# Kernel tuning notes

Hardware: AMD Instinct MI355X
Metric: run time of the kernel (lower is better)

## Reference

```python
import jax, jax.numpy as jnp
import numpy as np

N, IN_F, OUT_F = 8192, 4096, 4096
QMIN, QMAX = -128, 127  # int8 range for bitwidth 8


def setup_inputs() -> dict:
    key = jax.random.key(0)
    k1, k2, k3, k4 = jax.random.split(key, 4)
    x = jax.random.randint(k1, (N, IN_F), QMIN, QMAX + 1, dtype=jnp.int32).astype(jnp.int8)
    weight = jax.random.randint(k2, (OUT_F, IN_F), QMIN, QMAX + 1, dtype=jnp.int32).astype(jnp.int8)
    bias = jax.random.randint(k3, (OUT_F,), -1024, 1024, dtype=jnp.int32)
    weight_scale = jax.random.uniform(k4, (OUT_F,), dtype=jnp.float32, minval=0.001, maxval=0.02)
    input_scale = jnp.asarray([0.05], dtype=jnp.float32)
    output_scale = jnp.asarray([0.1], dtype=jnp.float32)
    output_zero_point = 0
    return {"x": x, "weight": weight, "bias": bias, "weight_scale": weight_scale,
            "input_scale": input_scale, "output_scale": output_scale,
            "output_zero_point": output_zero_point}


def reference(x, weight, bias, weight_scale, input_scale, output_scale, output_zero_point):
    # int32-accumulated GEMM with bias (CPU path of the torch module)
    acc = jnp.matmul(x.astype(jnp.int32), weight.astype(jnp.int32).T) + bias[None, :]  # [N, OUT_F] int32
    # fused dequant/requant epilogue
    scale_factor = (input_scale * weight_scale / output_scale)[None, :]  # [1, OUT_F]
    out = acc.astype(jnp.float32) * scale_factor + output_zero_point
    out = jnp.clip(jnp.round(out), QMIN, QMAX).astype(jnp.int8)
    return out
```

## Files before the change

### kernel.cpp

```cpp
#include <hip/hip_runtime.h>
#include <stdint.h>


#define M_DIM 8192
#define N_DIM 4096
#define K_DIM 4096
#define BM 256
#define BN 256
#define NKT2 (K_DIM / 32)
#define NBLK ((M_DIM / BM) * (N_DIM / BN))
#define ABUF (BM * 64)
#define BBUF (BN * 64)

using i32x4  = __attribute__((ext_vector_type(4))) int;
using i32x16 = __attribute__((ext_vector_type(16))) int;

typedef const __attribute__((address_space(1))) uint32_t* gptr_t;
typedef __attribute__((address_space(3))) uint32_t* lptr_t;

__device__ __forceinline__ void gload_lds16(const void* g, void* l) {
    __builtin_amdgcn_global_load_lds((gptr_t)g, (lptr_t)l, 16, 0, 0);
}

__device__ __forceinline__ int pack4(i32x4 v) {
    return (int)(((unsigned)v.x & 0xFFu) | (((unsigned)v.y & 0xFFu) << 8) |
                 (((unsigned)v.z & 0xFFu) << 16) | (((unsigned)v.w) << 24));
}

__global__ void pack_panels32_kernel(const int* __restrict__ src, int8_t* __restrict__ dst,
                                     int n_blocks) {
    int gid = blockIdx.x * blockDim.x + threadIdx.x;
    int blk = gid >> 6;
    int l = gid & 63;
    if (blk >= n_blocks) return;
    int rb = blk >> 7;
    int kt = blk & (NKT2 - 1);
    const i32x4* s4 = (const i32x4*)(src + (size_t)(rb * 32 + (l & 31)) * K_DIM
                                         + kt * 32 + (l >> 5) * 16);
    i32x4 o;
    o.x = pack4(s4[0]); o.y = pack4(s4[1]); o.z = pack4(s4[2]); o.w = pack4(s4[3]);
    *(i32x4*)(dst + (size_t)blk * 1024 + l * 16) = o;
}

#define MFMA32(a, b, c) __builtin_amdgcn_mfma_i32_32x32x32_i8((a), (b), (c), 0, 0, 0)

#define DSR(dst, base, off) \
    asm volatile("ds_read_b128 %0, %1 offset:%2" : "=&v"(dst) : "v"(base), "i"(off))

#define READ12(NS, SOFF)                                                        \
    DSR(fA[NS][0][0], aA, (SOFF) + 0);    DSR(fA[NS][0][1], aA, (SOFF) + 2048); \
    DSR(fA[NS][0][2], aA, (SOFF) + 4096); DSR(fA[NS][0][3], aA, (SOFF) + 6144); \
    DSR(fA[NS][1][0], aA, (SOFF) + 1024); DSR(fA[NS][1][1], aA, (SOFF) + 3072); \
    DSR(fA[NS][1][2], aA, (SOFF) + 5120); DSR(fA[NS][1][3], aA, (SOFF) + 7168); \
    DSR(fB[NS][0][0], aB, (SOFF) + 0);    DSR(fB[NS][0][1], aB, (SOFF) + 2048); \
    DSR(fB[NS][1][0], aB, (SOFF) + 1024); DSR(fB[NS][1][1], aB, (SOFF) + 3072);

#define MFMA_HALF(CS, K)                                                          \
    acc[0][0] = MFMA32(fA[CS][K][0], fB[CS][K][0], acc[0][0]);                    \
    acc[0][1] = MFMA32(fA[CS][K][0], fB[CS][K][1], acc[0][1]);                    \
    acc[1][0] = MFMA32(fA[CS][K][1], fB[CS][K][0], acc[1][0]);                    \
    acc[1][1] = MFMA32(fA[CS][K][1], fB[CS][K][1], acc[1][1]);                    \
    acc[2][0] = MFMA32(fA[CS][K][2], fB[CS][K][0], acc[2][0]);                    \
    acc[2][1] = MFMA32(fA[CS][K][2], fB[CS][K][1], acc[2][1]);                    \
    acc[3][0] = MFMA32(fA[CS][K][3], fB[CS][K][0], acc[3][0]);                    \
    acc[3][1] = MFMA32(fA[CS][K][3], fB[CS][K][1], acc[3][1]);

#define STAGE(SLOT)                                                     \
    gload_lds16(AgS,        ldsA + (SLOT) * ABUF + waoff);              \
    gload_lds16(AgS + 1024, ldsA + (SLOT) * ABUF + waoff + 1024);       \
    gload_lds16(BgS,        ldsB + (SLOT) * BBUF + waoff);              \
    gload_lds16(BgS + 1024, ldsB + (SLOT) * BBUF + waoff + 1024);       \
    AgS += 2048; BgS += 2048;

#define TILE_FULL(SLOT_STG, SOFF_NXT, NS, CS)                           \
  { STAGE(SLOT_STG)                                                     \
    asm volatile("s_waitcnt vmcnt(4)" ::: "memory");                    \
    __builtin_amdgcn_s_barrier();                                       \
    READ12(NS, SOFF_NXT)                                                \
    asm volatile("s_waitcnt lgkmcnt(12)" ::: "memory");                 \
    __builtin_amdgcn_sched_barrier(0);                                  \
    __builtin_amdgcn_s_setprio(1);                                      \
    MFMA_HALF(CS, 0)                                                    \
    MFMA_HALF(CS, 1)                                                    \
    __builtin_amdgcn_s_setprio(0); }

__global__ __launch_bounds__(512, 2)
void qgemm32_kernel(const int8_t* __restrict__ xp, const int8_t* __restrict__ wp,
                    const int* __restrict__ bias, const float* __restrict__ wscale,
                    const float* __restrict__ iscale, const float* __restrict__ oscale,
                    const int* __restrict__ zp, int* __restrict__ out) {
    extern __shared__ int8_t lds[];
    int8_t* ldsA = lds;
    int8_t* ldsB = lds + 4 * ABUF;

    const int tid  = threadIdx.x;
    const int wave = tid >> 6;
    const int lane = tid & 63;

    int b = blockIdx.x;
    int s = (b & 7) * (NBLK >> 3) + (b >> 3);
    const int bcol = (s & 15) * BN;
    const int brow = (s >> 4) * BM;

    const int wr = wave >> 2;
    const int wc = wave & 3;

    const int rb0 = brow >> 5;
    const int cb0 = bcol >> 5;
    const int8_t* AgS = xp + ((size_t)(rb0 + wave) * NKT2) * 1024 + lane * 16;
    const int8_t* BgS = wp + ((size_t)(cb0 + wave) * NKT2) * 1024 + lane * 16;
    const int waoff = wave * 2048;

    const unsigned aA = (unsigned)(uintptr_t)(ldsA + wr * 8192 + lane * 16);
    const unsigned aB = (unsigned)(uintptr_t)(ldsB + wc * 4096 + lane * 16);

    i32x16 acc[4][2] = {};
    i32x4 fA[2][2][4];
    i32x4 fB[2][2][2];

    STAGE(0)
    STAGE(1)
    asm volatile("s_waitcnt vmcnt(4)" ::: "memory");
    __builtin_amdgcn_s_barrier();
    READ12(0, 0)

    for (int i = 0; i < 15; ++i) {
        TILE_FULL(2, 16384, 1, 0)
        TILE_FULL(3, 32768, 0, 1)
        TILE_FULL(0, 49152, 1, 0)
        TILE_FULL(1,     0, 0, 1)
    }
    TILE_FULL(2, 16384, 1, 0)
    TILE_FULL(3, 32768, 0, 1)
    {
        asm volatile("s_waitcnt vmcnt(0)" ::: "memory");
        __builtin_amdgcn_s_barrier();
        READ12(1, 49152)
        asm volatile("s_waitcnt lgkmcnt(12)" ::: "memory");
        __builtin_amdgcn_sched_barrier(0);
        __builtin_amdgcn_s_setprio(1);
        MFMA_HALF(0, 0)
        MFMA_HALF(0, 1)
        __builtin_amdgcn_s_setprio(0);
    }
    asm volatile("s_waitcnt lgkmcnt(0)" ::: "memory");
    __builtin_amdgcn_sched_barrier(0);
    MFMA_HALF(1, 0)
    MFMA_HALF(1, 1)

    const float is_v = iscale[0];
    const float os_v = oscale[0];
    const float zpf = (float)zp[0];
    #pragma unroll
    for (int c = 0; c < 2; c++) {
        int col = bcol + wc * 64 + c * 32 + (lane & 31);
        float sf = (is_v * wscale[col]) / os_v;
        int bz = bias[col];
        #pragma unroll
        for (int r = 0; r < 4; r++) {
            int rowb = brow + wr * 128 + r * 32 + 4 * (lane >> 5);
            #pragma unroll
            for (int reg = 0; reg < 16; reg++) {
                int row = rowb + (reg & 3) + 8 * (reg >> 2);
                float v = (float)(acc[r][c][reg] + bz) * sf + zpf;
                v = rintf(v);
                v = fminf(fmaxf(v, -128.0f), 127.0f);
                out[(size_t)row * N_DIM + col] = (int)v;
            }
        }
    }
}

#define MFMA_I8(a, b, c) __builtin_amdgcn_mfma_i32_16x16x64_i8((a), (b), (c), 0, 0, 0)

__global__ void qgemm_fallback(const int* __restrict__ x32, const int* __restrict__ w32,
                               const int* __restrict__ bias, const float* __restrict__ wscale,
                               const float* __restrict__ iscale, const float* __restrict__ oscale,
                               const int* __restrict__ zp, int* __restrict__ out) {
    __shared__ int8_t As[128][64];
    __shared__ int8_t Bs[128][64];
    const int tid  = threadIdx.x;
    const int wave = tid >> 6;
    const int lane = tid & 63;
    int b = blockIdx.x;
    int s = (b & 7) * (gridDim.x >> 3) + (b >> 3);
    const int bcol = (s & 31) * 128;
    const int brow = (s >> 5) * 128;
    const int wr = wave >> 1;
    const int wc = wave & 1;
    i32x4 acc[4][4] = {};
    for (int kt = 0; kt < K_DIM; kt += 64) {
        int row = tid >> 1;
        int h = tid & 1;
        const i32x4* sa = (const i32x4*)(x32 + (size_t)(brow + row) * K_DIM + kt + h * 32);
        const i32x4* sb = (const i32x4*)(w32 + (size_t)(bcol + row) * K_DIM + kt + h * 32);
        int pa[8], pb[8];
        #pragma unroll
        for (int j = 0; j < 8; j++) { pa[j] = pack4(sa[j]); pb[j] = pack4(sb[j]); }
        *(i32x4*)&As[row][h * 32]      = *(i32x4*)&pa[0];
        *(i32x4*)&As[row][h * 32 + 16] = *(i32x4*)&pa[4];
        *(i32x4*)&Bs[row][h * 32]      = *(i32x4*)&pb[0];
        *(i32x4*)&Bs[row][h * 32 + 16] = *(i32x4*)&pb[4];
        __syncthreads();
        i32x4 a_frag[4], b_frag[4];
        #pragma unroll
        for (int m = 0; m < 4; m++)
            a_frag[m] = *(const i32x4*)&As[wr * 64 + m * 16 + (lane & 15)][(lane >> 4) * 16];
        #pragma unroll
        for (int n = 0; n < 4; n++)
            b_frag[n] = *(const i32x4*)&Bs[wc * 64 + n * 16 + (lane & 15)][(lane >> 4) * 16];
        #pragma unroll
        for (int m = 0; m < 4; m++)
            #pragma unroll
            for (int n = 0; n < 4; n++)
                acc[m][n] = MFMA_I8(a_frag[m], b_frag[n], acc[m][n]);
        __syncthreads();
    }
    const float is_v = iscale[0];
    const float os_v = oscale[0];
    const float zpf = (float)zp[0];
    #pragma unroll
    for (int n = 0; n < 4; n++) {
        int col = bcol + wc * 64 + n * 16 + (lane & 15);
        float sf = (is_v * wscale[col]) / os_v;
        int bz = bias[col];
        #pragma unroll
        for (int m = 0; m < 4; m++) {
            int row0 = brow + wr * 64 + m * 16 + (lane >> 4) * 4;
            #pragma unroll
            for (int r = 0; r < 4; r++) {
                float v = (float)(acc[m][n][r] + bz) * sf + zpf;
                v = rintf(v);
                v = fminf(fmaxf(v, -128.0f), 127.0f);
                out[(size_t)(row0 + r) * N_DIM + col] = (int)v;
            }
        }
    }
}

extern "C" void kernel_launch(void* const* d_in, const int* in_sizes, int n_in,
                              void* d_out, int out_size, void* d_ws, size_t ws_size,
                              hipStream_t stream) {
    const int*   x32    = (const int*)d_in[0];
    const int*   w32    = (const int*)d_in[1];
    const int*   bias   = (const int*)d_in[2];
    const float* wscale = (const float*)d_in[3];
    const float* iscale = (const float*)d_in[4];
    const float* oscale = (const float*)d_in[5];
    const int*   zp     = (const int*)d_in[6];
    int* out = (int*)d_out;

    const size_t need = (size_t)M_DIM * K_DIM + (size_t)N_DIM * K_DIM;
    const size_t lds_bytes = 4 * (size_t)(ABUF + BBUF);

    if (ws_size >= need) {
        int8_t* xp = (int8_t*)d_ws;
        int8_t* wp = xp + (size_t)M_DIM * K_DIM;
        const int nblkA = (M_DIM / 32) * NKT2;
        const int nblkB = (N_DIM / 32) * NKT2;
        pack_panels32_kernel<<<nblkA / 4, 256, 0, stream>>>(x32, xp, nblkA);
        pack_panels32_kernel<<<nblkB / 4, 256, 0, stream>>>(w32, wp, nblkB);
        (void)hipFuncSetAttribute((const void*)qgemm32_kernel,
                                  hipFuncAttributeMaxDynamicSharedMemorySize,
                                  (int)lds_bytes);
        qgemm32_kernel<<<NBLK, 512, lds_bytes, stream>>>(xp, wp, bias, wscale, iscale, oscale, zp, out);
    } else {
        qgemm_fallback<<<2048, 256, 0, stream>>>(x32, w32, bias, wscale, iscale, oscale, zp, out);
    }
}
```

Baseline: 183.3 us.

## Load B fragments straight from global into registers, bypassing LDS

The weight (B) operand is no longer staged through LDS. Each wave now issues global_load_dwordx4 directly into its fB fragment registers, one tile ahead, while A keeps its 4-slot global-to-LDS pipeline. This halves LDS use and drops the B ds_reads and their LDS bandwidth. In exchange, B global traffic is duplicated across the two wave rows that share a column. B load latency is hidden by only one tile of MFMA work, and register pressure rises.

```diff
diff --git a/kernel.cpp b/kernel.cpp
--- a/kernel.cpp
+++ b/kernel.cpp
@@ -10,7 +10,6 @@
 #define NKT2 (K_DIM / 32)
 #define NBLK ((M_DIM / BM) * (N_DIM / BN))
 #define ABUF (BM * 64)
-#define BBUF (BN * 64)
 
 using i32x4  = __attribute__((ext_vector_type(4))) int;
 using i32x16 = __attribute__((ext_vector_type(16))) int;
@@ -47,13 +46,20 @@
 #define DSR(dst, base, off) \
     asm volatile("ds_read_b128 %0, %1 offset:%2" : "=&v"(dst) : "v"(base), "i"(off))
 
-#define READ12(NS, SOFF)                                                        \
+#define GLB16(dst, addr, off) \
+    asm volatile("global_load_dwordx4 %0, %1, off offset:%2" \
+                 : "=&v"(dst) : "v"(addr), "i"(off))
+
+#define READ8(NS, SOFF)                                                         \
     DSR(fA[NS][0][0], aA, (SOFF) + 0);    DSR(fA[NS][0][1], aA, (SOFF) + 2048); \
     DSR(fA[NS][0][2], aA, (SOFF) + 4096); DSR(fA[NS][0][3], aA, (SOFF) + 6144); \
     DSR(fA[NS][1][0], aA, (SOFF) + 1024); DSR(fA[NS][1][1], aA, (SOFF) + 3072); \
-    DSR(fA[NS][1][2], aA, (SOFF) + 5120); DSR(fA[NS][1][3], aA, (SOFF) + 7168); \
-    DSR(fB[NS][0][0], aB, (SOFF) + 0);    DSR(fB[NS][0][1], aB, (SOFF) + 2048); \
-    DSR(fB[NS][1][0], aB, (SOFF) + 1024); DSR(fB[NS][1][1], aB, (SOFF) + 3072);
+    DSR(fA[NS][1][2], aA, (SOFF) + 5120); DSR(fA[NS][1][3], aA, (SOFF) + 7168);
+
+#define LOADB(NS)                                                       \
+    GLB16(fB[NS][0][0], Bg0, 0);    GLB16(fB[NS][1][0], Bg0, 1024);     \
+    GLB16(fB[NS][0][1], Bg1, 0);    GLB16(fB[NS][1][1], Bg1, 1024);     \
+    Bg0 += 2048; Bg1 += 2048;
 
 #define MFMA_HALF(CS, K)                                                          \
     acc[0][0] = MFMA32(fA[CS][K][0], fB[CS][K][0], acc[0][0]);                    \
@@ -65,19 +71,18 @@
     acc[3][0] = MFMA32(fA[CS][K][3], fB[CS][K][0], acc[3][0]);                    \
     acc[3][1] = MFMA32(fA[CS][K][3], fB[CS][K][1], acc[3][1]);
 
-#define STAGE(SLOT)                                                     \
+#define STAGE_A(SLOT)                                                   \
     gload_lds16(AgS,        ldsA + (SLOT) * ABUF + waoff);              \
     gload_lds16(AgS + 1024, ldsA + (SLOT) * ABUF + waoff + 1024);       \
-    gload_lds16(BgS,        ldsB + (SLOT) * BBUF + waoff);              \
-    gload_lds16(BgS + 1024, ldsB + (SLOT) * BBUF + waoff + 1024);       \
-    AgS += 2048; BgS += 2048;
+    AgS += 2048;
 
 #define TILE_FULL(SLOT_STG, SOFF_NXT, NS, CS)                           \
-  { STAGE(SLOT_STG)                                                     \
-    asm volatile("s_waitcnt vmcnt(4)" ::: "memory");                    \
+  { STAGE_A(SLOT_STG)                                                   \
+    LOADB(NS)                                                           \
+    asm volatile("s_waitcnt vmcnt(6)" ::: "memory");                    \
     __builtin_amdgcn_s_barrier();                                       \
-    READ12(NS, SOFF_NXT)                                                \
-    asm volatile("s_waitcnt lgkmcnt(12)" ::: "memory");                 \
+    READ8(NS, SOFF_NXT)                                                 \
+    asm volatile("s_waitcnt lgkmcnt(8)" ::: "memory");                  \
     __builtin_amdgcn_sched_barrier(0);                                  \
     __builtin_amdgcn_s_setprio(1);                                      \
     MFMA_HALF(CS, 0)                                                    \
@@ -91,7 +96,6 @@
                     const int* __restrict__ zp, int* __restrict__ out) {
     extern __shared__ int8_t lds[];
     int8_t* ldsA = lds;
-    int8_t* ldsB = lds + 4 * ABUF;
 
     const int tid  = threadIdx.x;
     const int wave = tid >> 6;
@@ -108,21 +112,23 @@
     const int rb0 = brow >> 5;
     const int cb0 = bcol >> 5;
     const int8_t* AgS = xp + ((size_t)(rb0 + wave) * NKT2) * 1024 + lane * 16;
-    const int8_t* BgS = wp + ((size_t)(cb0 + wave) * NKT2) * 1024 + lane * 16;
     const int waoff = wave * 2048;
 
+    const int8_t* Bg0 = wp + ((size_t)(cb0 + wc * 2)     * NKT2) * 1024 + lane * 16;
+    const int8_t* Bg1 = wp + ((size_t)(cb0 + wc * 2 + 1) * NKT2) * 1024 + lane * 16;
+
     const unsigned aA = (unsigned)(uintptr_t)(ldsA + wr * 8192 + lane * 16);
-    const unsigned aB = (unsigned)(uintptr_t)(ldsB + wc * 4096 + lane * 16);
 
     i32x16 acc[4][2] = {};
     i32x4 fA[2][2][4];
     i32x4 fB[2][2][2];
 
-    STAGE(0)
-    STAGE(1)
-    asm volatile("s_waitcnt vmcnt(4)" ::: "memory");
+    STAGE_A(0)
+    STAGE_A(1)
+    LOADB(0)
+    asm volatile("s_waitcnt vmcnt(0)" ::: "memory");
     __builtin_amdgcn_s_barrier();
-    READ12(0, 0)
+    READ8(0, 0)
 
     for (int i = 0; i < 15; ++i) {
         TILE_FULL(2, 16384, 1, 0)
@@ -133,16 +139,18 @@
     TILE_FULL(2, 16384, 1, 0)
     TILE_FULL(3, 32768, 0, 1)
     {
-        asm volatile("s_waitcnt vmcnt(0)" ::: "memory");
+        LOADB(1)
+        asm volatile("s_waitcnt vmcnt(4)" ::: "memory");
         __builtin_amdgcn_s_barrier();
-        READ12(1, 49152)
-        asm volatile("s_waitcnt lgkmcnt(12)" ::: "memory");
+        READ8(1, 49152)
+        asm volatile("s_waitcnt lgkmcnt(8)" ::: "memory");
         __builtin_amdgcn_sched_barrier(0);
         __builtin_amdgcn_s_setprio(1);
         MFMA_HALF(0, 0)
         MFMA_HALF(0, 1)
         __builtin_amdgcn_s_setprio(0);
     }
+    asm volatile("s_waitcnt vmcnt(0)" ::: "memory");
     asm volatile("s_waitcnt lgkmcnt(0)" ::: "memory");
     __builtin_amdgcn_sched_barrier(0);
     MFMA_HALF(1, 0)
@@ -251,7 +259,7 @@
     int* out = (int*)d_out;
 
     const size_t need = (size_t)M_DIM * K_DIM + (size_t)N_DIM * K_DIM;
-    const size_t lds_bytes = 4 * (size_t)(ABUF + BBUF);
+    const size_t lds_bytes = 4 * (size_t)ABUF;
 
     if (ws_size >= need) {
         int8_t* xp = (int8_t*)d_ws;
```

Result: slower. 187.2 us (+2.2%).

## Use 4 waves per block with 128x128 warp tiles instead of 8 waves

Applied to the files above, without the earlier changes.

Cuts the GEMM block from 8 waves to 4 and gives each wave a 128x128 output tile (4x4 MFMA 32x32 accumulators) instead of 128x64. Each wave now stages two 32-row panels of A and of B per K step, and the LDS slot addresses are precomputed. The goal is more MFMA work per LDS fragment read (16 reads feed 32 MFMAs versus 12 feeding 16). In exchange the accumulators double to 256 VGPRs per lane, there are fewer waves to hide latency, and the launch bound drops to one block per CU.

```diff
diff --git a/kernel.cpp b/kernel.cpp
--- a/kernel.cpp
+++ b/kernel.cpp
@@ -9,8 +9,7 @@
 #define BN 256
 #define NKT2 (K_DIM / 32)
 #define NBLK ((M_DIM / BM) * (N_DIM / BN))
-#define ABUF (BM * 64)
-#define BBUF (BN * 64)
+#define SLOT 16384
 
 using i32x4  = __attribute__((ext_vector_type(4))) int;
 using i32x16 = __attribute__((ext_vector_type(16))) int;
@@ -47,51 +46,65 @@
 #define DSR(dst, base, off) \
     asm volatile("ds_read_b128 %0, %1 offset:%2" : "=&v"(dst) : "v"(base), "i"(off))
 
-#define READ12(NS, SOFF)                                                        \
-    DSR(fA[NS][0][0], aA, (SOFF) + 0);    DSR(fA[NS][0][1], aA, (SOFF) + 2048); \
-    DSR(fA[NS][0][2], aA, (SOFF) + 4096); DSR(fA[NS][0][3], aA, (SOFF) + 6144); \
-    DSR(fA[NS][1][0], aA, (SOFF) + 1024); DSR(fA[NS][1][1], aA, (SOFF) + 3072); \
-    DSR(fA[NS][1][2], aA, (SOFF) + 5120); DSR(fA[NS][1][3], aA, (SOFF) + 7168); \
-    DSR(fB[NS][0][0], aB, (SOFF) + 0);    DSR(fB[NS][0][1], aB, (SOFF) + 2048); \
-    DSR(fB[NS][1][0], aB, (SOFF) + 1024); DSR(fB[NS][1][1], aB, (SOFF) + 3072);
-
-#define MFMA_HALF(CS, K)                                                          \
-    acc[0][0] = MFMA32(fA[CS][K][0], fB[CS][K][0], acc[0][0]);                    \
-    acc[0][1] = MFMA32(fA[CS][K][0], fB[CS][K][1], acc[0][1]);                    \
-    acc[1][0] = MFMA32(fA[CS][K][1], fB[CS][K][0], acc[1][0]);                    \
-    acc[1][1] = MFMA32(fA[CS][K][1], fB[CS][K][1], acc[1][1]);                    \
-    acc[2][0] = MFMA32(fA[CS][K][2], fB[CS][K][0], acc[2][0]);                    \
-    acc[2][1] = MFMA32(fA[CS][K][2], fB[CS][K][1], acc[2][1]);                    \
-    acc[3][0] = MFMA32(fA[CS][K][3], fB[CS][K][0], acc[3][0]);                    \
-    acc[3][1] = MFMA32(fA[CS][K][3], fB[CS][K][1], acc[3][1]);
-
-#define STAGE(SLOT)                                                     \
-    gload_lds16(AgS,        ldsA + (SLOT) * ABUF + waoff);              \
-    gload_lds16(AgS + 1024, ldsA + (SLOT) * ABUF + waoff + 1024);       \
-    gload_lds16(BgS,        ldsB + (SLOT) * BBUF + waoff);              \
-    gload_lds16(BgS + 1024, ldsB + (SLOT) * BBUF + waoff + 1024);       \
-    AgS += 2048; BgS += 2048;
-
-#define TILE_FULL(SLOT_STG, SOFF_NXT, NS, CS)                           \
-  { STAGE(SLOT_STG)                                                     \
-    asm volatile("s_waitcnt vmcnt(4)" ::: "memory");                    \
+#define READ16(NS, AB, BB)                                              \
+    DSR(fA[NS][0][0], AB, 0);    DSR(fA[NS][0][1], AB, 2048);           \
+    DSR(fA[NS][0][2], AB, 4096); DSR(fA[NS][0][3], AB, 6144);           \
+    DSR(fA[NS][1][0], AB, 1024); DSR(fA[NS][1][1], AB, 3072);           \
+    DSR(fA[NS][1][2], AB, 5120); DSR(fA[NS][1][3], AB, 7168);           \
+    DSR(fB[NS][0][0], BB, 0);    DSR(fB[NS][0][1], BB, 2048);           \
+    DSR(fB[NS][0][2], BB, 4096); DSR(fB[NS][0][3], BB, 6144);           \
+    DSR(fB[NS][1][0], BB, 1024); DSR(fB[NS][1][1], BB, 3072);           \
+    DSR(fB[NS][1][2], BB, 5120); DSR(fB[NS][1][3], BB, 7168);
+
+#define MFMA_K(CS, K)                                                   \
+    acc[0][0] = MFMA32(fA[CS][K][0], fB[CS][K][0], acc[0][0]);          \
+    acc[0][1] = MFMA32(fA[CS][K][0], fB[CS][K][1], acc[0][1]);          \
+    acc[0][2] = MFMA32(fA[CS][K][0], fB[CS][K][2], acc[0][2]);          \
+    acc[0][3] = MFMA32(fA[CS][K][0], fB[CS][K][3], acc[0][3]);          \
+    acc[1][0] = MFMA32(fA[CS][K][1], fB[CS][K][0], acc[1][0]);          \
+    acc[1][1] = MFMA32(fA[CS][K][1], fB[CS][K][1], acc[1][1]);          \
+    acc[1][2] = MFMA32(fA[CS][K][1], fB[CS][K][2], acc[1][2]);          \
+    acc[1][3] = MFMA32(fA[CS][K][1], fB[CS][K][3], acc[1][3]);          \
+    acc[2][0] = MFMA32(fA[CS][K][2], fB[CS][K][0], acc[2][0]);          \
+    acc[2][1] = MFMA32(fA[CS][K][2], fB[CS][K][1], acc[2][1]);          \
+    acc[2][2] = MFMA32(fA[CS][K][2], fB[CS][K][2], acc[2][2]);          \
+    acc[2][3] = MFMA32(fA[CS][K][2], fB[CS][K][3], acc[2][3]);          \
+    acc[3][0] = MFMA32(fA[CS][K][3], fB[CS][K][0], acc[3][0]);          \
+    acc[3][1] = MFMA32(fA[CS][K][3], fB[CS][K][1], acc[3][1]);          \
+    acc[3][2] = MFMA32(fA[CS][K][3], fB[CS][K][2], acc[3][2]);          \
+    acc[3][3] = MFMA32(fA[CS][K][3], fB[CS][K][3], acc[3][3]);
+
+#define STAGE8(S)                                                               \
+    gload_lds16(AgS,         ldsA + (S) * SLOT + (2 * wave) * 2048);            \
+    gload_lds16(AgS  + 1024, ldsA + (S) * SLOT + (2 * wave) * 2048 + 1024);     \
+    gload_lds16(AgS2,        ldsA + (S) * SLOT + (2 * wave + 1) * 2048);        \
+    gload_lds16(AgS2 + 1024, ldsA + (S) * SLOT + (2 * wave + 1) * 2048 + 1024); \
+    gload_lds16(BgS,         ldsB + (S) * SLOT + (2 * wave) * 2048);            \
+    gload_lds16(BgS  + 1024, ldsB + (S) * SLOT + (2 * wave) * 2048 + 1024);     \
+    gload_lds16(BgS2,        ldsB + (S) * SLOT + (2 * wave + 1) * 2048);        \
+    gload_lds16(BgS2 + 1024, ldsB + (S) * SLOT + (2 * wave + 1) * 2048 + 1024); \
+    AgS += 2048; AgS2 += 2048; BgS += 2048; BgS2 += 2048;
+
+#define TILE_FULL(SS, AB, BB, NS, CS)                                   \
+  { STAGE8(SS)                                                          \
+    asm volatile("s_waitcnt vmcnt(8)" ::: "memory");                    \
     __builtin_amdgcn_s_barrier();                                       \
-    READ12(NS, SOFF_NXT)                                                \
-    asm volatile("s_waitcnt lgkmcnt(12)" ::: "memory");                 \
+    READ16(NS, AB, BB)                                                  \
+    asm volatile("s_waitcnt lgkmcnt(15)" ::: "memory");                 \
     __builtin_amdgcn_sched_barrier(0);                                  \
     __builtin_amdgcn_s_setprio(1);                                      \
-    MFMA_HALF(CS, 0)                                                    \
-    MFMA_HALF(CS, 1)                                                    \
+    MFMA_K(CS, 0)                                                       \
+    MFMA_K(CS, 1)                                                       \
     __builtin_amdgcn_s_setprio(0); }
 
-__global__ __launch_bounds__(512, 2)
+__global__ __launch_bounds__(256, 1)
 void qgemm32_kernel(const int8_t* __restrict__ xp, const int8_t* __restrict__ wp,
                     const int* __restrict__ bias, const float* __restrict__ wscale,
                     const float* __restrict__ iscale, const float* __restrict__ oscale,
                     const int* __restrict__ zp, int* __restrict__ out) {
     extern __shared__ int8_t lds[];
     int8_t* ldsA = lds;
-    int8_t* ldsB = lds + 4 * ABUF;
+    int8_t* ldsB = lds + 4 * SLOT;
 
     const int tid  = threadIdx.x;
     const int wave = tid >> 6;
@@ -102,58 +115,61 @@
     const int bcol = (s & 15) * BN;
     const int brow = (s >> 4) * BM;
 
-    const int wr = wave >> 2;
-    const int wc = wave & 3;
+    const int wr = wave >> 1;
+    const int wc = wave & 1;
 
     const int rb0 = brow >> 5;
     const int cb0 = bcol >> 5;
-    const int8_t* AgS = xp + ((size_t)(rb0 + wave) * NKT2) * 1024 + lane * 16;
-    const int8_t* BgS = wp + ((size_t)(cb0 + wave) * NKT2) * 1024 + lane * 16;
-    const int waoff = wave * 2048;
-
-    const unsigned aA = (unsigned)(uintptr_t)(ldsA + wr * 8192 + lane * 16);
-    const unsigned aB = (unsigned)(uintptr_t)(ldsB + wc * 4096 + lane * 16);
-
-    i32x16 acc[4][2] = {};
+    const int8_t* AgS  = xp + ((size_t)(rb0 + 2 * wave)     * NKT2) * 1024 + lane * 16;
+    const int8_t* AgS2 = xp + ((size_t)(rb0 + 2 * wave + 1) * NKT2) * 1024 + lane * 16;
+    const int8_t* BgS  = wp + ((size_t)(cb0 + 2 * wave)     * NKT2) * 1024 + lane * 16;
+    const int8_t* BgS2 = wp + ((size_t)(cb0 + 2 * wave + 1) * NKT2) * 1024 + lane * 16;
+
+    const unsigned aA0 = (unsigned)(uintptr_t)(ldsA + wr * 8192 + lane * 16);
+    const unsigned aA1 = aA0 + SLOT, aA2 = aA0 + 2 * SLOT, aA3 = aA0 + 3 * SLOT;
+    const unsigned aB0 = (unsigned)(uintptr_t)(ldsB + wc * 8192 + lane * 16);
+    const unsigned aB1 = aB0 + SLOT, aB2 = aB0 + 2 * SLOT, aB3 = aB0 + 3 * SLOT;
+
+    i32x16 acc[4][4] = {};
     i32x4 fA[2][2][4];
-    i32x4 fB[2][2][2];
-
-    STAGE(0)
-    STAGE(1)
-    asm volatile("s_waitcnt vmcnt(4)" ::: "memory");
+    i32x4 fB[2][2][4];
+
+    STAGE8(0)
+    STAGE8(1)
+    asm volatile("s_waitcnt vmcnt(8)" ::: "memory");
     __builtin_amdgcn_s_barrier();
-    READ12(0, 0)
+    READ16(0, aA0, aB0)
 
     for (int i = 0; i < 15; ++i) {
-        TILE_FULL(2, 16384, 1, 0)
-        TILE_FULL(3, 32768, 0, 1)
-        TILE_FULL(0, 49152, 1, 0)
-        TILE_FULL(1,     0, 0, 1)
-    }
-    TILE_FULL(2, 16384, 1, 0)
-    TILE_FULL(3, 32768, 0, 1)
+        TILE_FULL(2, aA1, aB1, 1, 0)
+        TILE_FULL(3, aA2, aB2, 0, 1)
+        TILE_FULL(0, aA3, aB3, 1, 0)
+        TILE_FULL(1, aA0, aB0, 0, 1)
+    }
+    TILE_FULL(2, aA1, aB1, 1, 0)
+    TILE_FULL(3, aA2, aB2, 0, 1)
     {
         asm volatile("s_waitcnt vmcnt(0)" ::: "memory");
         __builtin_amdgcn_s_barrier();
-        READ12(1, 49152)
-        asm volatile("s_waitcnt lgkmcnt(12)" ::: "memory");
+        READ16(1, aA3, aB3)
+        asm volatile("s_waitcnt lgkmcnt(15)" ::: "memory");
         __builtin_amdgcn_sched_barrier(0);
         __builtin_amdgcn_s_setprio(1);
-        MFMA_HALF(0, 0)
-        MFMA_HALF(0, 1)
+        MFMA_K(0, 0)
+        MFMA_K(0, 1)
         __builtin_amdgcn_s_setprio(0);
     }
     asm volatile("s_waitcnt lgkmcnt(0)" ::: "memory");
     __builtin_amdgcn_sched_barrier(0);
-    MFMA_HALF(1, 0)
-    MFMA_HALF(1, 1)
+    MFMA_K(1, 0)
+    MFMA_K(1, 1)
 
     const float is_v = iscale[0];
     const float os_v = oscale[0];
     const float zpf = (float)zp[0];
     #pragma unroll
-    for (int c = 0; c < 2; c++) {
-        int col = bcol + wc * 64 + c * 32 + (lane & 31);
+    for (int c = 0; c < 4; c++) {
+        int col = bcol + wc * 128 + c * 32 + (lane & 31);
         float sf = (is_v * wscale[col]) / os_v;
         int bz = bias[col];
         #pragma unroll
@@ -251,7 +267,7 @@
     int* out = (int*)d_out;
 
     const size_t need = (size_t)M_DIM * K_DIM + (size_t)N_DIM * K_DIM;
-    const size_t lds_bytes = 4 * (size_t)(ABUF + BBUF);
+    const size_t lds_bytes = 8 * (size_t)SLOT;
 
     if (ws_size >= need) {
         int8_t* xp = (int8_t*)d_ws;
@@ -263,7 +279,7 @@
         (void)hipFuncSetAttribute((const void*)qgemm32_kernel,
                                   hipFuncAttributeMaxDynamicSharedMemorySize,
                                   (int)lds_bytes);
-        qgemm32_kernel<<<NBLK, 512, lds_bytes, stream>>>(xp, wp, bias, wscale, iscale, oscale, zp, out);
+        qgemm32_kernel<<<NBLK, 256, lds_bytes, stream>>>(xp, wp, bias, wscale, iscale, oscale, zp, out);
     } else {
         qgemm_fallback<<<2048, 256, 0, stream>>>(x32, w32, bias, wscale, iscale, oscale, zp, out);
     }
```

Result: no change. 184.1 us (+0.5%).
